# Kernel optimization log

Measured on AMD Instinct MI355X. Metric: run time of the kernel, lower is better.

## Reference

```python
import jax, jax.numpy as jnp
import numpy as np

ORDER = 4


def setup_inputs() -> dict:
    key = jax.random.key(0)
    k1, k2, k3, k4 = jax.random.split(key, 4)
    B, IN, OUT = 8192, 1024, 1024
    x = jax.random.normal(k1, (B, IN), dtype=jnp.float32)
    base_weight = jax.random.normal(k2, (OUT, IN), dtype=jnp.float32) * (1.0 / np.sqrt(IN))
    std = 1.0 / (IN * np.sqrt(ORDER))
    taylor_coeffs = jax.random.normal(k3, (OUT, IN, ORDER), dtype=jnp.float32) * std
    bound = 1.0 / np.sqrt(IN)
    bias = jax.random.uniform(k4, (OUT,), dtype=jnp.float32, minval=-bound, maxval=bound)
    return {"x": x, "base_weight": base_weight, "taylor_coeffs": taylor_coeffs, "bias": bias}


def reference(x, base_weight, taylor_coeffs, bias):
    # base path: SiLU(x) @ W^T
    base_out = jnp.einsum('bi,oi->bo', jax.nn.silu(x), base_weight)
    # taylor path: x_powers[b,i,k] = x**k, k=0..ORDER-1; contract with coeffs[o,i,k]
    powers = jnp.arange(ORDER, dtype=x.dtype)  # [K]
    x_powers = x[:, :, None] ** powers  # [B, IN, K]
    taylor_out = jnp.einsum('bik,oik->bo', x_powers, taylor_coeffs)
    return base_out + taylor_out + bias
```

## Files before the change

kernel.cpp:

```cpp
#include <hip/hip_runtime.h>
#include <hip/hip_bf16.h>

#define GLOBAL_AS __attribute__((address_space(1)))
#define LDS_AS    __attribute__((address_space(3)))

typedef __bf16 bf16x8 __attribute__((ext_vector_type(8)));
typedef float  f32x4  __attribute__((ext_vector_type(4)));

constexpr int BATCH = 8192;
constexpr int IN    = 1024;
constexpr int OUT   = 1024;
constexpr int KDIM  = IN * 4;
constexpr int BM = 128, BN = 256, BK = 64;
constexpr int NKT  = KDIM / BK;
constexpr int LDSBUF = 24576;

__device__ __forceinline__ unsigned short f2bf(float f) {
    union { float f; unsigned u; } v; v.f = f;
    unsigned r = v.u + 0x7fffu + ((v.u >> 16) & 1u);
    return (unsigned short)(r >> 16);
}
__device__ __forceinline__ unsigned pk(unsigned short a, unsigned short b) {
    return (unsigned)a | ((unsigned)b << 16);
}

__global__ __launch_bounds__(256) void prep(const float* __restrict__ x,
                                            const float* __restrict__ W,
                                            const float* __restrict__ C,
                                            const float* __restrict__ bias,
                                            unsigned short* __restrict__ Ab,
                                            unsigned short* __restrict__ Bb,
                                            float* __restrict__ be) {
    if (blockIdx.x < 8192) {
        int idx = blockIdx.x * 256 + threadIdx.x;
        float4 v = reinterpret_cast<const float4*>(x)[idx];
        float e0[4] = {v.x, v.y, v.z, v.w};
        unsigned short o[16];
#pragma unroll
        for (int j = 0; j < 4; ++j) {
            float xv = e0[j];
            float s  = xv / (1.0f + __expf(-xv));
            float x2 = xv * xv;
            o[4*j+0] = f2bf(s);
            o[4*j+1] = f2bf(xv);
            o[4*j+2] = f2bf(x2);
            o[4*j+3] = f2bf(x2 * xv);
        }
        uint4 d0 = make_uint4(pk(o[0],o[1]), pk(o[2],o[3]),   pk(o[4],o[5]),   pk(o[6],o[7]));
        uint4 d1 = make_uint4(pk(o[8],o[9]), pk(o[10],o[11]), pk(o[12],o[13]), pk(o[14],o[15]));
        uint4* dst = reinterpret_cast<uint4*>(Ab) + (size_t)idx * 2;
        dst[0] = d0;
        dst[1] = d1;
    } else {
        const int o = blockIdx.x - 8192, t = threadIdx.x;
        const int i0 = t * 4;
        const float4* c4 = reinterpret_cast<const float4*>(C + ((size_t)o * IN + i0) * 4);
        float4 w4 = *reinterpret_cast<const float4*>(W + (size_t)o * IN + i0);
        float wv[4] = {w4.x, w4.y, w4.z, w4.w};
        float s = 0.f;
        unsigned d[8];
#pragma unroll
        for (int j = 0; j < 4; ++j) {
            float4 c = c4[j];
            s += c.x;
            d[2*j]   = pk(f2bf(wv[j]), f2bf(c.y));
            d[2*j+1] = pk(f2bf(c.z),   f2bf(c.w));
        }
        uint4* dst = reinterpret_cast<uint4*>(Bb + (size_t)o * KDIM + i0 * 4);
        dst[0] = make_uint4(d[0], d[1], d[2], d[3]);
        dst[1] = make_uint4(d[4], d[5], d[6], d[7]);
#pragma unroll
        for (int off = 32; off > 0; off >>= 1) s += __shfl_down(s, off, 64);
        __shared__ float red[4];
        if ((t & 63) == 0) red[t >> 6] = s;
        __syncthreads();
        if (t == 0) be[o] = bias[o] + red[0] + red[1] + red[2] + red[3];
    }
}

__global__ __launch_bounds__(512, 2) void gemm_kan(
        const unsigned short* __restrict__ Ab,
        const unsigned short* __restrict__ Bb,
        const float* __restrict__ be,
        float* __restrict__ out) {
    extern __shared__ unsigned short smem[];

    const int t    = threadIdx.x;
    const int l    = blockIdx.x;
    const int bm   = l & 63;
    const int bn   = l >> 6;
    const int lane = t & 63;
    const int wave = t >> 6;
    const int wr   = wave >> 2;
    const int wc   = wave & 3;
    const int l15  = lane & 15;
    const int quad = lane >> 4;
    const int x7   = l15 & 7;

    const unsigned short* aP[2];
    const unsigned short* bP[4];
#pragma unroll
    for (int i = 0; i < 2; ++i) {
        int ch = i * 512 + t, r = ch >> 3, g = (ch & 7) ^ (r & 7);
        aP[i] = Ab + (size_t)(bm * BM + r) * KDIM + g * 8;
    }
#pragma unroll
    for (int i = 0; i < 4; ++i) {
        int ch = i * 512 + t, r = ch >> 3, g = (ch & 7) ^ (r & 7);
        bP[i] = Bb + (size_t)(bn * BN + r) * KDIM + g * 8;
    }

    const int aRd = (wr * 32 + l15) * 64;
    const int bRd = 8192 + (wc * 64 + l15) * 64;

    f32x4 acc[4][4];
    const f32x4 zero = {0.f, 0.f, 0.f, 0.f};
#pragma unroll
    for (int i = 0; i < 4; ++i)
#pragma unroll
        for (int j = 0; j < 4; ++j) acc[i][j] = zero;

#define STAGE(tile, buf) do {                                                          \
    _Pragma("unroll")                                                                  \
    for (int i_ = 0; i_ < 2; ++i_)                                                     \
        __builtin_amdgcn_global_load_lds(                                              \
            (const GLOBAL_AS void*)(aP[i_] + (size_t)(tile) * BK),                     \
            (LDS_AS void*)(smem + (buf) * LDSBUF + (i_ * 512 + t) * 8), 16, 0, 0);     \
    _Pragma("unroll")                                                                  \
    for (int i_ = 0; i_ < 4; ++i_)                                                     \
        __builtin_amdgcn_global_load_lds(                                              \
            (const GLOBAL_AS void*)(bP[i_] + (size_t)(tile) * BK),                     \
            (LDS_AS void*)(smem + (buf) * LDSBUF + 8192 + (i_ * 512 + t) * 8),         \
            16, 0, 0);                                                                 \
} while (0)

    STAGE(0, 0);
    STAGE(1, 1);
    asm volatile("s_waitcnt vmcnt(6)" ::: "memory");
    __builtin_amdgcn_s_barrier();

    int cb = 0;
    for (int kt = 0; kt < NKT; ++kt) {
        const unsigned short* sb = smem + cb * LDSBUF;
        const int nb = (cb >= 1) ? cb - 1 : 2;

        if (kt + 2 < NKT) STAGE(kt + 2, nb);

#pragma unroll
        for (int kk = 0; kk < 2; ++kk) {
            const int ck = ((kk * 4 + quad) ^ x7) * 8;
            bf16x8 af[4], bv[4];
            af[0] = *reinterpret_cast<const bf16x8*>(sb + aRd + ck);
            af[1] = *reinterpret_cast<const bf16x8*>(sb + aRd + 1024 + ck);
            af[2] = *reinterpret_cast<const bf16x8*>(sb + aRd + 4096 + ck);
            af[3] = *reinterpret_cast<const bf16x8*>(sb + aRd + 5120 + ck);
#pragma unroll
            for (int ni = 0; ni < 4; ++ni)
                bv[ni] = *reinterpret_cast<const bf16x8*>(sb + bRd + ni * 1024 + ck);
#pragma unroll
            for (int mi = 0; mi < 4; ++mi)
#pragma unroll
                for (int ni = 0; ni < 4; ++ni)
                    acc[mi][ni] = __builtin_amdgcn_mfma_f32_16x16x32_bf16(
                        af[mi], bv[ni], acc[mi][ni], 0, 0, 0);
        }

        if (kt < NKT - 2) {
            asm volatile("s_waitcnt vmcnt(6)" ::: "memory");
            __builtin_amdgcn_s_barrier();
        } else if (kt == NKT - 2) {
            asm volatile("s_waitcnt vmcnt(0)" ::: "memory");
            __builtin_amdgcn_s_barrier();
        }
        cb = (cb == 2) ? 0 : cb + 1;
    }

#undef STAGE

    float bev[4];
#pragma unroll
    for (int ni = 0; ni < 4; ++ni)
        bev[ni] = be[bn * BN + wc * 64 + ni * 16 + l15];

#pragma unroll
    for (int mg = 0; mg < 4; ++mg) {
        const int grow = bm * BM + (mg >> 1) * 64 + wr * 32 + (mg & 1) * 16 + quad * 4;
#pragma unroll
        for (int ni = 0; ni < 4; ++ni) {
            const int gcol = bn * BN + wc * 64 + ni * 16 + l15;
            float* po = out + (size_t)grow * OUT + gcol;
#pragma unroll
            for (int r = 0; r < 4; ++r)
                po[(size_t)r * OUT] = acc[mg][ni][r] + bev[ni];
        }
    }
}

extern "C" void kernel_launch(void* const* d_in, const int* in_sizes, int n_in,
                              void* d_out, int out_size, void* d_ws, size_t ws_size,
                              hipStream_t stream) {
    const float* x    = (const float*)d_in[0];
    const float* W    = (const float*)d_in[1];
    const float* C    = (const float*)d_in[2];
    const float* bias = (const float*)d_in[3];
    float* out = (float*)d_out;

    unsigned short* Ab = (unsigned short*)d_ws;
    unsigned short* Bb = Ab + (size_t)BATCH * KDIM;
    float*          be = (float*)(Bb + (size_t)OUT * KDIM);

    constexpr int LDS_BYTES = 3 * LDSBUF * 2;
    static bool inited = false;
    if (!inited) {
        hipFuncSetAttribute(reinterpret_cast<const void*>(&gemm_kan),
                            hipFuncAttributeMaxDynamicSharedMemorySize, LDS_BYTES);
        inited = true;
    }

    prep<<<dim3(8192 + 1024), dim3(256), 0, stream>>>(x, W, C, bias, Ab, Bb, be);

    gemm_kan<<<dim3(256), dim3(512), LDS_BYTES, stream>>>(Ab, Bb, be, out);
}
```

Before: 173.2 us.

## Fuse activation expansion of x into GEMM A-tile staging

Drops the separate pass that expanded x into a bf16 [silu, x, x^2, x^3] matrix in global memory. Each GEMM workgroup now loads raw fp32 x one tile ahead, computes the expansion in registers and writes it swizzled into LDS, while B still uses async global-to-LDS loads. This removes a 64MB write and re-read of the expanded A matrix. In exchange, every column block recomputes the expansion (4x redundant), adds VALU and exp work plus LDS stores inside the main loop, and changes the waitcnt accounting.

```diff
diff --git a/kernel.cpp b/kernel.cpp
--- a/kernel.cpp
+++ b/kernel.cpp
@@ -24,62 +24,38 @@
     return (unsigned)a | ((unsigned)b << 16);
 }
 
-__global__ __launch_bounds__(256) void prep(const float* __restrict__ x,
-                                            const float* __restrict__ W,
-                                            const float* __restrict__ C,
-                                            const float* __restrict__ bias,
-                                            unsigned short* __restrict__ Ab,
-                                            unsigned short* __restrict__ Bb,
-                                            float* __restrict__ be) {
-    if (blockIdx.x < 8192) {
-        int idx = blockIdx.x * 256 + threadIdx.x;
-        float4 v = reinterpret_cast<const float4*>(x)[idx];
-        float e0[4] = {v.x, v.y, v.z, v.w};
-        unsigned short o[16];
-#pragma unroll
-        for (int j = 0; j < 4; ++j) {
-            float xv = e0[j];
-            float s  = xv / (1.0f + __expf(-xv));
-            float x2 = xv * xv;
-            o[4*j+0] = f2bf(s);
-            o[4*j+1] = f2bf(xv);
-            o[4*j+2] = f2bf(x2);
-            o[4*j+3] = f2bf(x2 * xv);
-        }
-        uint4 d0 = make_uint4(pk(o[0],o[1]), pk(o[2],o[3]),   pk(o[4],o[5]),   pk(o[6],o[7]));
-        uint4 d1 = make_uint4(pk(o[8],o[9]), pk(o[10],o[11]), pk(o[12],o[13]), pk(o[14],o[15]));
-        uint4* dst = reinterpret_cast<uint4*>(Ab) + (size_t)idx * 2;
-        dst[0] = d0;
-        dst[1] = d1;
-    } else {
-        const int o = blockIdx.x - 8192, t = threadIdx.x;
-        const int i0 = t * 4;
-        const float4* c4 = reinterpret_cast<const float4*>(C + ((size_t)o * IN + i0) * 4);
-        float4 w4 = *reinterpret_cast<const float4*>(W + (size_t)o * IN + i0);
-        float wv[4] = {w4.x, w4.y, w4.z, w4.w};
-        float s = 0.f;
-        unsigned d[8];
-#pragma unroll
-        for (int j = 0; j < 4; ++j) {
-            float4 c = c4[j];
-            s += c.x;
-            d[2*j]   = pk(f2bf(wv[j]), f2bf(c.y));
-            d[2*j+1] = pk(f2bf(c.z),   f2bf(c.w));
-        }
-        uint4* dst = reinterpret_cast<uint4*>(Bb + (size_t)o * KDIM + i0 * 4);
-        dst[0] = make_uint4(d[0], d[1], d[2], d[3]);
-        dst[1] = make_uint4(d[4], d[5], d[6], d[7]);
-#pragma unroll
-        for (int off = 32; off > 0; off >>= 1) s += __shfl_down(s, off, 64);
-        __shared__ float red[4];
-        if ((t & 63) == 0) red[t >> 6] = s;
-        __syncthreads();
-        if (t == 0) be[o] = bias[o] + red[0] + red[1] + red[2] + red[3];
-    }
+__global__ __launch_bounds__(256) void prep_b(const float* __restrict__ W,
+                                              const float* __restrict__ C,
+                                              const float* __restrict__ bias,
+                                              unsigned short* __restrict__ Bb,
+                                              float* __restrict__ be) {
+    const int o = blockIdx.x, t = threadIdx.x;
+    const int i0 = t * 4;
+    const float4* c4 = reinterpret_cast<const float4*>(C + ((size_t)o * IN + i0) * 4);
+    float4 w4 = *reinterpret_cast<const float4*>(W + (size_t)o * IN + i0);
+    float wv[4] = {w4.x, w4.y, w4.z, w4.w};
+    float s = 0.f;
+    unsigned d[8];
+#pragma unroll
+    for (int j = 0; j < 4; ++j) {
+        float4 c = c4[j];
+        s += c.x;
+        d[2*j]   = pk(f2bf(wv[j]), f2bf(c.y));
+        d[2*j+1] = pk(f2bf(c.z),   f2bf(c.w));
+    }
+    uint4* dst = reinterpret_cast<uint4*>(Bb + (size_t)o * KDIM + i0 * 4);
+    dst[0] = make_uint4(d[0], d[1], d[2], d[3]);
+    dst[1] = make_uint4(d[4], d[5], d[6], d[7]);
+#pragma unroll
+    for (int off = 32; off > 0; off >>= 1) s += __shfl_down(s, off, 64);
+    __shared__ float red[4];
+    if ((t & 63) == 0) red[t >> 6] = s;
+    __syncthreads();
+    if (t == 0) be[o] = bias[o] + red[0] + red[1] + red[2] + red[3];
 }
 
 __global__ __launch_bounds__(512, 2) void gemm_kan(
-        const unsigned short* __restrict__ Ab,
+        const float* __restrict__ x,
         const unsigned short* __restrict__ Bb,
         const float* __restrict__ be,
         float* __restrict__ out) {
@@ -97,19 +73,20 @@
     const int quad = lane >> 4;
     const int x7   = l15 & 7;
 
-    const unsigned short* aP[2];
     const unsigned short* bP[4];
-#pragma unroll
-    for (int i = 0; i < 2; ++i) {
-        int ch = i * 512 + t, r = ch >> 3, g = (ch & 7) ^ (r & 7);
-        aP[i] = Ab + (size_t)(bm * BM + r) * KDIM + g * 8;
-    }
 #pragma unroll
     for (int i = 0; i < 4; ++i) {
         int ch = i * 512 + t, r = ch >> 3, g = (ch & 7) ^ (r & 7);
         bP[i] = Bb + (size_t)(bn * BN + r) * KDIM + g * 8;
     }
 
+    const int arow  = t >> 2;
+    const int axi   = t & 3;
+    const int aoff0 = arow * 64 + (((axi * 2)     ^ (arow & 7)) * 8);
+    const int aoff1 = arow * 64 + (((axi * 2 + 1) ^ (arow & 7)) * 8);
+    const float4* xp = reinterpret_cast<const float4*>(
+        x + (size_t)(bm * BM + arow) * IN + axi * 4);
+
     const int aRd = (wr * 32 + l15) * 64;
     const int bRd = 8192 + (wc * 64 + l15) * 64;
 
@@ -120,12 +97,7 @@
 #pragma unroll
         for (int j = 0; j < 4; ++j) acc[i][j] = zero;
 
-#define STAGE(tile, buf) do {                                                          \
-    _Pragma("unroll")                                                                  \
-    for (int i_ = 0; i_ < 2; ++i_)                                                     \
-        __builtin_amdgcn_global_load_lds(                                              \
-            (const GLOBAL_AS void*)(aP[i_] + (size_t)(tile) * BK),                     \
-            (LDS_AS void*)(smem + (buf) * LDSBUF + (i_ * 512 + t) * 8), 16, 0, 0);     \
+#define STAGE_B(tile, buf) do {                                                        \
     _Pragma("unroll")                                                                  \
     for (int i_ = 0; i_ < 4; ++i_)                                                     \
         __builtin_amdgcn_global_load_lds(                                              \
@@ -134,9 +106,35 @@
             16, 0, 0);                                                                 \
 } while (0)
 
-    STAGE(0, 0);
-    STAGE(1, 1);
-    asm volatile("s_waitcnt vmcnt(6)" ::: "memory");
+#define STAGE_A(buf, v) do {                                                           \
+    float e_[4] = {(v).x, (v).y, (v).z, (v).w};                                        \
+    unsigned short o_[16];                                                             \
+    _Pragma("unroll")                                                                  \
+    for (int j = 0; j < 4; ++j) {                                                      \
+        float xv_ = e_[j];                                                             \
+        float s_  = xv_ / (1.0f + __expf(-xv_));                                       \
+        float x2_ = xv_ * xv_;                                                         \
+        o_[4*j+0] = f2bf(s_);                                                          \
+        o_[4*j+1] = f2bf(xv_);                                                         \
+        o_[4*j+2] = f2bf(x2_);                                                         \
+        o_[4*j+3] = f2bf(x2_ * xv_);                                                   \
+    }                                                                                  \
+    unsigned short* ab_ = smem + (buf) * LDSBUF;                                       \
+    *reinterpret_cast<uint4*>(ab_ + aoff0) =                                           \
+        make_uint4(pk(o_[0],o_[1]), pk(o_[2],o_[3]), pk(o_[4],o_[5]), pk(o_[6],o_[7]));\
+    *reinterpret_cast<uint4*>(ab_ + aoff1) =                                           \
+        make_uint4(pk(o_[8],o_[9]), pk(o_[10],o_[11]), pk(o_[12],o_[13]), pk(o_[14],o_[15]));\
+} while (0)
+
+    float4 xa   = xp[0];
+    float4 xb   = xp[4];
+    float4 xcur = xp[8];
+    float4 xnext = xcur;
+    STAGE_B(0, 0);
+    STAGE_B(1, 1);
+    STAGE_A(0, xa);
+    STAGE_A(1, xb);
+    asm volatile("s_waitcnt vmcnt(4) lgkmcnt(0)" ::: "memory");
     __builtin_amdgcn_s_barrier();
 
     int cb = 0;
@@ -144,7 +142,8 @@
         const unsigned short* sb = smem + cb * LDSBUF;
         const int nb = (cb >= 1) ? cb - 1 : 2;
 
-        if (kt + 2 < NKT) STAGE(kt + 2, nb);
+        if (kt + 3 < NKT) xnext = xp[(kt + 3) * 4];
+        if (kt + 2 < NKT) STAGE_B(kt + 2, nb);
 
 #pragma unroll
         for (int kk = 0; kk < 2; ++kk) {
@@ -165,17 +164,26 @@
                         af[mi], bv[ni], acc[mi][ni], 0, 0, 0);
         }
 
-        if (kt < NKT - 2) {
-            asm volatile("s_waitcnt vmcnt(6)" ::: "memory");
+        if (kt + 2 < NKT) {
+            STAGE_A(nb, xcur);
+            xcur = xnext;
+        }
+
+        if (kt < NKT - 3) {
+            asm volatile("s_waitcnt vmcnt(5) lgkmcnt(0)" ::: "memory");
+            __builtin_amdgcn_s_barrier();
+        } else if (kt == NKT - 3) {
+            asm volatile("s_waitcnt vmcnt(4) lgkmcnt(0)" ::: "memory");
             __builtin_amdgcn_s_barrier();
         } else if (kt == NKT - 2) {
-            asm volatile("s_waitcnt vmcnt(0)" ::: "memory");
+            asm volatile("s_waitcnt vmcnt(0) lgkmcnt(0)" ::: "memory");
             __builtin_amdgcn_s_barrier();
         }
         cb = (cb == 2) ? 0 : cb + 1;
     }
 
-#undef STAGE
+#undef STAGE_A
+#undef STAGE_B
 
     float bev[4];
 #pragma unroll
@@ -205,8 +213,7 @@
     const float* bias = (const float*)d_in[3];
     float* out = (float*)d_out;
 
-    unsigned short* Ab = (unsigned short*)d_ws;
-    unsigned short* Bb = Ab + (size_t)BATCH * KDIM;
+    unsigned short* Bb = (unsigned short*)d_ws;
     float*          be = (float*)(Bb + (size_t)OUT * KDIM);
 
     constexpr int LDS_BYTES = 3 * LDSBUF * 2;
@@ -217,7 +224,7 @@
         inited = true;
     }
 
-    prep<<<dim3(8192 + 1024), dim3(256), 0, stream>>>(x, W, C, bias, Ab, Bb, be);
-
-    gemm_kan<<<dim3(256), dim3(512), LDS_BYTES, stream>>>(Ab, Bb, be, out);
-}
+    prep_b<<<dim3(1024), dim3(256), 0, stream>>>(W, C, bias, Bb, be);
+
+    gemm_kan<<<dim3(256), dim3(512), LDS_BYTES, stream>>>(x, Bb, be, out);
+}
```

Result: no change. 173.3 us (+0.0%).
